# Performance work log

Hardware: AMD Instinct MI355X
Metric: run time of the kernel (lower is better)

The kernel has to match this reference:

```python
import jax, jax.numpy as jnp
import numpy as np

B, N, D, H = 2, 2048, 1024, 16
DH = D // H  # 64


def setup_inputs() -> dict:
    key = jax.random.key(0)
    k1, k2, k3, k4, k5 = jax.random.split(key, 5)
    x = jax.random.normal(k1, (B, N, D), dtype=jnp.float32)
    # per-head kqv Linear weights, stacked: [H, D, 3*DH] (acts as x @ W)
    W_kqv = jax.random.normal(k2, (H, D, 3 * DH), dtype=jnp.float32) * 0.02
    b_kqv = jax.random.normal(k3, (H, 3 * DH), dtype=jnp.float32) * 0.02
    W_proj = jax.random.normal(k4, (D, D), dtype=jnp.float32) * 0.02
    b_proj = jax.random.normal(k5, (D,), dtype=jnp.float32) * 0.02
    return {"x": x, "W_kqv": W_kqv, "b_kqv": b_kqv, "W_proj": W_proj, "b_proj": b_proj}


def reference(x, W_kqv, b_kqv, W_proj, b_proj):
    # per-head projections, all heads batched: [B, H, N, 3*DH]
    kqv = jnp.einsum('bnd,hde->bhne', x, W_kqv) + b_kqv[None, :, None, :]
    # original chunk order is k, q, v
    k, q, v = jnp.split(kqv, 3, axis=-1)  # each [B, H, N, DH]
    # scores: A = q @ k^T / sqrt(DH)  -> [B, H, N, N]
    A = jnp.einsum('bhnd,bhmd->bhnm', q, k) / jnp.sqrt(jnp.asarray(DH, x.dtype))
    causal = jnp.tril(jnp.ones((N, N), dtype=bool))
    A = jnp.where(causal[None, None, :, :], A, -jnp.inf)
    attn = jax.nn.softmax(A, axis=-1)
    sa = jnp.einsum('bhnm,bhmd->bhnd', attn, v)          # [B, H, N, DH]
    sa = sa.transpose(0, 2, 1, 3).reshape(B, N, D)        # concat heads
    out = sa @ W_proj.T + b_proj                          # output projection
    return out
```

## Files before the change

kernel.cpp:

```cpp
#include <hip/hip_runtime.h>
#include <hip/hip_bf16.h>
#include <cstdint>
#include <cstddef>

#define B_  2
#define N_  2048
#define D_  1024
#define H_  16
#define DH_ 64
#define E3_ 192

typedef __attribute__((ext_vector_type(8))) short short8;
typedef __attribute__((ext_vector_type(8))) unsigned short ushort8v;
typedef __attribute__((ext_vector_type(4))) float floatx4;

static __device__ __forceinline__ unsigned short f2bf(float f) {
  union { float f; unsigned u; } c; c.f = f;
  unsigned r = c.u + 0x7fffu + ((c.u >> 16) & 1u);
  return (unsigned short)(r >> 16);
}

#define MFMA(a,b,c) __builtin_amdgcn_mfma_f32_16x16x32_bf16((a),(b),(c),0,0,0)

#define GL_LDS16(g, l) __builtin_amdgcn_global_load_lds( \
    (const __attribute__((address_space(1))) void*)(g),  \
    (__attribute__((address_space(3))) void*)(l), 16, 0, 0)

__global__ __launch_bounds__(256) void k_f2bf(const float* __restrict__ in,
                                              unsigned short* __restrict__ out, int n8) {
  int i = blockIdx.x * blockDim.x + threadIdx.x;
  if (i >= n8) return;
  const float4* p = (const float4*)in + (size_t)i * 2;
  float4 a = p[0], b = p[1];
  ushort8v o;
  o[0]=f2bf(a.x); o[1]=f2bf(a.y); o[2]=f2bf(a.z); o[3]=f2bf(a.w);
  o[4]=f2bf(b.x); o[5]=f2bf(b.y); o[6]=f2bf(b.z); o[7]=f2bf(b.w);
  *((ushort8v*)out + i) = o;
}

__global__ __launch_bounds__(256) void k_twkqv(const float* __restrict__ W,
                                               unsigned short* __restrict__ Wt) {
  __shared__ float tile[64][65];
  int h = blockIdx.z, cat = blockIdx.y, e0 = cat * 64, d0 = blockIdx.x * 64;
  int t = threadIdx.x;
  const float* Wp = W + (size_t)h * D_ * E3_;
  int dr = t >> 2, ec = (t & 3) * 16;
#pragma unroll
  for (int j = 0; j < 16; j += 4) {
    float4 wv = *(const float4*)&Wp[(size_t)(d0 + dr) * E3_ + e0 + ec + j];
    tile[dr][ec + j + 0] = wv.x; tile[dr][ec + j + 1] = wv.y;
    tile[dr][ec + j + 2] = wv.z; tile[dr][ec + j + 3] = wv.w;
  }
  __syncthreads();
  int er = t >> 2, dc = (t & 3) * 16;
  ushort8v o0, o1;
#pragma unroll
  for (int j = 0; j < 8; j++) o0[j] = f2bf(tile[dc + j][er]);
#pragma unroll
  for (int j = 0; j < 8; j++) o1[j] = f2bf(tile[dc + 8 + j][er]);
  size_t o = ((size_t)(cat * 1024 + h * 64 + er)) * D_ + d0 + dc;
  *(ushort8v*)&Wt[o]     = o0;
  *(ushort8v*)&Wt[o + 8] = o1;
}

__global__ __launch_bounds__(256) void k_qkv(const unsigned short* __restrict__ Xb,
                                             const unsigned short* __restrict__ Wt,
                                             const float* __restrict__ bkqv,
                                             unsigned short* __restrict__ Qb,
                                             unsigned short* __restrict__ Kb,
                                             unsigned short* __restrict__ Vt) {
  __shared__ unsigned short Alds[2][128 * 32];
  __shared__ unsigned short Blds[2][128 * 32];
  int t = threadIdx.x;
  int m0 = blockIdx.x * 128, c0 = blockIdx.y * 128;
  int wave = t >> 6, lane = t & 63, quad = lane >> 4, l16 = lane & 15;
  int wm = (wave >> 1) * 64, wn = (wave & 1) * 64;
  floatx4 acc[4][4];
#pragma unroll
  for (int i = 0; i < 4; i++)
#pragma unroll
    for (int j = 0; j < 4; j++) acc[i][j] = (floatx4){0.f, 0.f, 0.f, 0.f};

  const unsigned short* gA = Xb + (size_t)(m0 + wave * 32 + (lane >> 2)) * D_ + (lane & 3) * 8;
  const unsigned short* gB = Wt + (size_t)(c0 + wave * 32 + (lane >> 2)) * D_ + (lane & 3) * 8;
  unsigned short* lA0 = &Alds[0][(wave * 32) * 32];
  unsigned short* lA1 = &Alds[1][(wave * 32) * 32];
  unsigned short* lB0 = &Blds[0][(wave * 32) * 32];
  unsigned short* lB1 = &Blds[1][(wave * 32) * 32];

  for (int k0 = 0; k0 < D_; k0 += 64) {
    GL_LDS16(gA + k0,                 lA0);
    GL_LDS16(gA + k0 + 16 * D_,       lA0 + 16 * 32);
    GL_LDS16(gA + k0 + 32,            lA1);
    GL_LDS16(gA + k0 + 32 + 16 * D_,  lA1 + 16 * 32);
    GL_LDS16(gB + k0,                 lB0);
    GL_LDS16(gB + k0 + 16 * D_,       lB0 + 16 * 32);
    GL_LDS16(gB + k0 + 32,            lB1);
    GL_LDS16(gB + k0 + 32 + 16 * D_,  lB1 + 16 * 32);
    __syncthreads();
#pragma unroll
    for (int kk = 0; kk < 2; kk++) {
      short8 a[4], b[4];
#pragma unroll
      for (int mi = 0; mi < 4; mi++) a[mi] = *(const short8*)&Alds[kk][(wm + mi * 16 + l16) * 32 + quad * 8];
#pragma unroll
      for (int ni = 0; ni < 4; ni++) b[ni] = *(const short8*)&Blds[kk][(wn + ni * 16 + l16) * 32 + quad * 8];
#pragma unroll
      for (int mi = 0; mi < 4; mi++)
#pragma unroll
        for (int ni = 0; ni < 4; ni++) acc[mi][ni] = MFMA(a[mi], b[ni], acc[mi][ni]);
    }
    __syncthreads();
  }

  int cat = c0 >> 10;
#pragma unroll
  for (int mi = 0; mi < 4; mi++)
#pragma unroll
    for (int ni = 0; ni < 4; ni++) {
      int colp = c0 + wn + ni * 16 + l16;
      int h = (colp >> 6) & 15;
      int e = colp & 63;
      int grow = m0 + wm + mi * 16 + quad * 4;
      int b = grow >> 11, n0 = grow & (N_ - 1);
      int bh = b * H_ + h;
      float bias = bkqv[h * E3_ + cat * 64 + e];
      floatx4 v = acc[mi][ni];
      if (cat == 0) {
        size_t base = ((size_t)bh * N_ + n0) * DH_ + e;
#pragma unroll
        for (int r = 0; r < 4; r++) Kb[base + (size_t)r * DH_] = f2bf(v[r] + bias);
      } else if (cat == 1) {
        size_t base = ((size_t)bh * N_ + n0) * DH_ + e;
#pragma unroll
        for (int r = 0; r < 4; r++) Qb[base + (size_t)r * DH_] = f2bf((v[r] + bias) * 0.125f);
      } else {
        ushort4 pk;
        pk.x = f2bf(v[0] + bias); pk.y = f2bf(v[1] + bias);
        pk.z = f2bf(v[2] + bias); pk.w = f2bf(v[3] + bias);
        *(ushort4*)&Vt[((size_t)bh * DH_ + e) * N_ + n0] = pk;
      }
    }
}

#define PSTR 72
__global__ __launch_bounds__(256) void k_flash(const unsigned short* __restrict__ Qb,
                                               const unsigned short* __restrict__ Kb,
                                               const unsigned short* __restrict__ Vt,
                                               unsigned short* __restrict__ sab) {
  int bh = blockIdx.x;
  int yr = blockIdx.y, g = yr >> 3, o = yr & 7;
  int qb = (g == 0) ? o : (g == 1) ? 31 - o : (g == 2) ? 8 + o : 23 - o;
  int q0b = qb * 64;
  int wave = threadIdx.x >> 6;
  int lane = threadIdx.x & 63, quad = lane >> 4, l16 = lane & 15;
  const unsigned short* Qp = Qb + (size_t)bh * N_ * DH_;
  const unsigned short* Kp = Kb + (size_t)bh * N_ * DH_;
  const unsigned short* Vp = Vt + (size_t)bh * DH_ * N_;
  __shared__ unsigned short Klds[2][2 * 64 * 32];
  __shared__ unsigned short Vlds[2][2 * 64 * 32];
  __shared__ unsigned short Plds[4][16 * PSTR];
  unsigned short* P = Plds[wave];

  int q0w = q0b + wave * 16;
  short8 qf0 = *(const short8*)&Qp[(q0w + l16) * DH_ + quad * 8];
  short8 qf1 = *(const short8*)&Qp[(q0w + l16) * DH_ + 32 + quad * 8];

  const unsigned short* gK = Kp + (size_t)(wave * 16 + (lane >> 2)) * DH_ + (lane & 3) * 8;
  const unsigned short* gV = Vp + (size_t)(wave * 16 + (lane >> 2)) * N_ + (lane & 3) * 8;
  int lofs = (wave * 16) * 32;

  floatx4 O[4];
  float lr[4];
#pragma unroll
  for (int r = 0; r < 4; r++) { O[r] = (floatx4){0.f, 0.f, 0.f, 0.f}; lr[r] = 0.f; }

  int nt = (q0b >> 6) + 1;
  GL_LDS16(gK,      &Klds[0][lofs]);
  GL_LDS16(gK + 32, &Klds[0][lofs + 64 * 32]);
  GL_LDS16(gV,      &Vlds[0][lofs]);
  GL_LDS16(gV + 32, &Vlds[0][lofs + 64 * 32]);

  for (int i = 0; i < nt; i++) {
    int buf = i & 1;
    __syncthreads();
    if (i + 1 < nt) {
      int kvn = (i + 1) << 6;
      GL_LDS16(gK + (size_t)kvn * DH_,      &Klds[buf ^ 1][lofs]);
      GL_LDS16(gK + (size_t)kvn * DH_ + 32, &Klds[buf ^ 1][lofs + 64 * 32]);
      GL_LDS16(gV + kvn,                    &Vlds[buf ^ 1][lofs]);
      GL_LDS16(gV + kvn + 32,               &Vlds[buf ^ 1][lofs + 64 * 32]);
    }
    short8 kf[4][2], vf[4][2];
#pragma unroll
    for (int c = 0; c < 4; c++) {
      kf[c][0] = *(const short8*)&Klds[buf][(c * 16 + l16) * 32 + quad * 8];
      kf[c][1] = *(const short8*)&Klds[buf][(64 + c * 16 + l16) * 32 + quad * 8];
      vf[c][0] = *(const short8*)&Vlds[buf][(c * 16 + l16) * 32 + quad * 8];
      vf[c][1] = *(const short8*)&Vlds[buf][(64 + c * 16 + l16) * 32 + quad * 8];
    }
    floatx4 s[4];
#pragma unroll
    for (int c = 0; c < 4; c++) {
      s[c] = (floatx4){0.f, 0.f, 0.f, 0.f};
      s[c] = MFMA(qf0, kf[c][0], s[c]);
      s[c] = MFMA(qf1, kf[c][1], s[c]);
    }
    if (i == nt - 1) {
#pragma unroll
      for (int c = 0; c < 4; c++)
#pragma unroll
        for (int r = 0; r < 4; r++) {
          int row = wave * 16 + quad * 4 + r;
          if (c * 16 + l16 > row) s[c][r] = -1e30f;
        }
    }
#pragma unroll
    for (int c = 0; c < 4; c++)
#pragma unroll
      for (int r = 0; r < 4; r++)
        s[c][r] = __builtin_amdgcn_exp2f(s[c][r] * 1.44269504f);
#pragma unroll
    for (int r = 0; r < 4; r++)
      lr[r] += (s[0][r] + s[1][r]) + (s[2][r] + s[3][r]);
#pragma unroll
    for (int c = 0; c < 4; c++)
#pragma unroll
      for (int r = 0; r < 4; r++)
        P[(quad * 4 + r) * PSTR + c * 16 + l16] = f2bf(s[c][r]);
    __asm__ volatile("s_waitcnt lgkmcnt(0)" ::: "memory");
    short8 pa0 = *(const short8*)&P[l16 * PSTR + quad * 8];
    short8 pa1 = *(const short8*)&P[l16 * PSTR + 32 + quad * 8];
    __asm__ volatile("" ::: "memory");
#pragma unroll
    for (int dt = 0; dt < 4; dt++) {
      O[dt] = MFMA(pa0, vf[dt][0], O[dt]);
      O[dt] = MFMA(pa1, vf[dt][1], O[dt]);
    }
  }
#pragma unroll
  for (int m = 1; m < 16; m <<= 1)
#pragma unroll
    for (int r = 0; r < 4; r++) lr[r] += __shfl_xor(lr[r], m);

  int b = bh >> 4, h = bh & 15;
#pragma unroll
  for (int r = 0; r < 4; r++) {
    float inv = 1.0f / lr[r];
    size_t base = ((size_t)b * N_ + q0w + quad * 4 + r) * D_ + h * DH_;
#pragma unroll
    for (int dt = 0; dt < 4; dt++) sab[base + dt * 16 + l16] = f2bf(O[dt][r] * inv);
  }
}

__global__ __launch_bounds__(256) void k_proj(const unsigned short* __restrict__ sab,
                                              const unsigned short* __restrict__ Wpb,
                                              const float* __restrict__ bproj,
                                              float* __restrict__ out) {
  __shared__ unsigned short Alds[2][128 * 32];
  __shared__ unsigned short Blds[2][64 * 32];
  int t = threadIdx.x;
  int m0 = blockIdx.x * 128, c0 = blockIdx.y * 64;
  int wave = t >> 6, lane = t & 63, quad = lane >> 4, l16 = lane & 15;
  int wm = (wave >> 1) * 64, wn = (wave & 1) * 32;
  floatx4 acc[4][2];
#pragma unroll
  for (int i = 0; i < 4; i++) { acc[i][0] = (floatx4){0,0,0,0}; acc[i][1] = (floatx4){0,0,0,0}; }

  const unsigned short* gA = sab + (size_t)(m0 + wave * 32 + (lane >> 2)) * D_ + (lane & 3) * 8;
  const unsigned short* gB = Wpb + (size_t)(c0 + wave * 16 + (lane >> 2)) * D_ + (lane & 3) * 8;
  unsigned short* lA0 = &Alds[0][(wave * 32) * 32];
  unsigned short* lA1 = &Alds[1][(wave * 32) * 32];
  unsigned short* lB0 = &Blds[0][(wave * 16) * 32];
  unsigned short* lB1 = &Blds[1][(wave * 16) * 32];

  for (int k0 = 0; k0 < D_; k0 += 64) {
    GL_LDS16(gA + k0,                lA0);
    GL_LDS16(gA + k0 + 16 * D_,      lA0 + 16 * 32);
    GL_LDS16(gA + k0 + 32,           lA1);
    GL_LDS16(gA + k0 + 32 + 16 * D_, lA1 + 16 * 32);
    GL_LDS16(gB + k0,                lB0);
    GL_LDS16(gB + k0 + 32,           lB1);
    __syncthreads();
#pragma unroll
    for (int kk = 0; kk < 2; kk++) {
      short8 a[4], b[2];
#pragma unroll
      for (int mi = 0; mi < 4; mi++) a[mi] = *(const short8*)&Alds[kk][(wm + mi * 16 + l16) * 32 + quad * 8];
#pragma unroll
      for (int ni = 0; ni < 2; ni++) b[ni] = *(const short8*)&Blds[kk][(wn + ni * 16 + l16) * 32 + quad * 8];
#pragma unroll
      for (int mi = 0; mi < 4; mi++)
#pragma unroll
        for (int ni = 0; ni < 2; ni++) acc[mi][ni] = MFMA(a[mi], b[ni], acc[mi][ni]);
    }
    __syncthreads();
  }
#pragma unroll
  for (int mi = 0; mi < 4; mi++)
#pragma unroll
    for (int ni = 0; ni < 2; ni++) {
      int col = c0 + wn + ni * 16 + l16;
      int grow = m0 + wm + mi * 16 + quad * 4;
      float bias = bproj[col];
#pragma unroll
      for (int r = 0; r < 4; r++)
        out[(size_t)(grow + r) * D_ + col] = acc[mi][ni][r] + bias;
    }
}

extern "C" void kernel_launch(void* const* d_in, const int* in_sizes, int n_in,
                              void* d_out, int out_size, void* d_ws, size_t ws_size,
                              hipStream_t stream) {
  const float* x     = (const float*)d_in[0];
  const float* Wkqv  = (const float*)d_in[1];
  const float* bkqv  = (const float*)d_in[2];
  const float* Wproj = (const float*)d_in[3];
  const float* bproj = (const float*)d_in[4];
  float* out = (float*)d_out;

  char* w = (char*)d_ws;
  unsigned short* Xb  = (unsigned short*)(w);
  unsigned short* Wt  = (unsigned short*)(w + (8u  << 20));
  unsigned short* Wpb = (unsigned short*)(w + (14u << 20));
  unsigned short* Qb  = (unsigned short*)(w + (16u << 20));
  unsigned short* Kb  = (unsigned short*)(w + (24u << 20));
  unsigned short* Vt  = (unsigned short*)(w + (32u << 20));
  unsigned short* sa  = (unsigned short*)(w + (40u << 20));

  k_f2bf<<<(B_ * N_ * D_ / 8 + 255) / 256, 256, 0, stream>>>(x, Xb, B_ * N_ * D_ / 8);
  k_twkqv<<<dim3(D_ / 64, 3, H_), 256, 0, stream>>>(Wkqv, Wt);
  k_f2bf<<<(D_ * D_ / 8 + 255) / 256, 256, 0, stream>>>(Wproj, Wpb, D_ * D_ / 8);
  k_qkv<<<dim3(B_ * N_ / 128, 3072 / 128), 256, 0, stream>>>(Xb, Wt, bkqv, Qb, Kb, Vt);
  k_flash<<<dim3(B_ * H_, N_ / 64), 256, 0, stream>>>(Qb, Kb, Vt, sa);
  k_proj<<<dim3(B_ * N_ / 128, D_ / 64), 256, 0, stream>>>(sa, Wpb, bproj, out);
}
```

Baseline: 188.6 us.

## Merge prep kernels, double-buffer QKV and proj GEMM loads, shrink proj tiles

```diff
diff --git a/kernel.cpp b/kernel.cpp
--- a/kernel.cpp
+++ b/kernel.cpp
@@ -26,24 +26,30 @@
     (const __attribute__((address_space(1))) void*)(g),  \
     (__attribute__((address_space(3))) void*)(l), 16, 0, 0)
 
-__global__ __launch_bounds__(256) void k_f2bf(const float* __restrict__ in,
-                                              unsigned short* __restrict__ out, int n8) {
-  int i = blockIdx.x * blockDim.x + threadIdx.x;
-  if (i >= n8) return;
-  const float4* p = (const float4*)in + (size_t)i * 2;
-  float4 a = p[0], b = p[1];
-  ushort8v o;
-  o[0]=f2bf(a.x); o[1]=f2bf(a.y); o[2]=f2bf(a.z); o[3]=f2bf(a.w);
-  o[4]=f2bf(b.x); o[5]=f2bf(b.y); o[6]=f2bf(b.z); o[7]=f2bf(b.w);
-  *((ushort8v*)out + i) = o;
-}
-
-__global__ __launch_bounds__(256) void k_twkqv(const float* __restrict__ W,
-                                               unsigned short* __restrict__ Wt) {
+__global__ __launch_bounds__(256) void k_prep(const float* __restrict__ x,
+                                              const float* __restrict__ Wkqv,
+                                              const float* __restrict__ Wproj,
+                                              unsigned short* __restrict__ Xb,
+                                              unsigned short* __restrict__ Wt,
+                                              unsigned short* __restrict__ Wpb) {
   __shared__ float tile[64][65];
-  int h = blockIdx.z, cat = blockIdx.y, e0 = cat * 64, d0 = blockIdx.x * 64;
-  int t = threadIdx.x;
-  const float* Wp = W + (size_t)h * D_ * E3_;
+  int bx = blockIdx.x, t = threadIdx.x;
+  if (bx < 2048 || bx >= 2816) {
+    const float* in = (bx < 2048) ? x : Wproj;
+    unsigned short* out = (bx < 2048) ? Xb : Wpb;
+    int i = ((bx < 2048) ? bx : bx - 2816) * 256 + t;
+    const float4* p = (const float4*)in + (size_t)i * 2;
+    float4 a = p[0], b = p[1];
+    ushort8v o;
+    o[0]=f2bf(a.x); o[1]=f2bf(a.y); o[2]=f2bf(a.z); o[3]=f2bf(a.w);
+    o[4]=f2bf(b.x); o[5]=f2bf(b.y); o[6]=f2bf(b.z); o[7]=f2bf(b.w);
+    *((ushort8v*)out + i) = o;
+    return;
+  }
+  int idx = bx - 2048;
+  int d0 = (idx & 15) * 64, rem = idx >> 4;
+  int cat = rem % 3, h = rem / 3, e0 = cat * 64;
+  const float* Wp = Wkqv + (size_t)h * D_ * E3_;
   int dr = t >> 2, ec = (t & 3) * 16;
 #pragma unroll
   for (int j = 0; j < 16; j += 4) {
@@ -83,34 +89,32 @@
 
   const unsigned short* gA = Xb + (size_t)(m0 + wave * 32 + (lane >> 2)) * D_ + (lane & 3) * 8;
   const unsigned short* gB = Wt + (size_t)(c0 + wave * 32 + (lane >> 2)) * D_ + (lane & 3) * 8;
-  unsigned short* lA0 = &Alds[0][(wave * 32) * 32];
-  unsigned short* lA1 = &Alds[1][(wave * 32) * 32];
-  unsigned short* lB0 = &Blds[0][(wave * 32) * 32];
-  unsigned short* lB1 = &Blds[1][(wave * 32) * 32];
-
-  for (int k0 = 0; k0 < D_; k0 += 64) {
-    GL_LDS16(gA + k0,                 lA0);
-    GL_LDS16(gA + k0 + 16 * D_,       lA0 + 16 * 32);
-    GL_LDS16(gA + k0 + 32,            lA1);
-    GL_LDS16(gA + k0 + 32 + 16 * D_,  lA1 + 16 * 32);
-    GL_LDS16(gB + k0,                 lB0);
-    GL_LDS16(gB + k0 + 16 * D_,       lB0 + 16 * 32);
-    GL_LDS16(gB + k0 + 32,            lB1);
-    GL_LDS16(gB + k0 + 32 + 16 * D_,  lB1 + 16 * 32);
+  int lofs = (wave * 32) * 32;
+
+  GL_LDS16(gA,            &Alds[0][lofs]);
+  GL_LDS16(gA + 16 * D_,  &Alds[0][lofs + 16 * 32]);
+  GL_LDS16(gB,            &Blds[0][lofs]);
+  GL_LDS16(gB + 16 * D_,  &Blds[0][lofs + 16 * 32]);
+
+  for (int i = 0; i < 32; i++) {
+    int buf = i & 1;
     __syncthreads();
-#pragma unroll
-    for (int kk = 0; kk < 2; kk++) {
-      short8 a[4], b[4];
-#pragma unroll
-      for (int mi = 0; mi < 4; mi++) a[mi] = *(const short8*)&Alds[kk][(wm + mi * 16 + l16) * 32 + quad * 8];
-#pragma unroll
-      for (int ni = 0; ni < 4; ni++) b[ni] = *(const short8*)&Blds[kk][(wn + ni * 16 + l16) * 32 + quad * 8];
-#pragma unroll
-      for (int mi = 0; mi < 4; mi++)
-#pragma unroll
-        for (int ni = 0; ni < 4; ni++) acc[mi][ni] = MFMA(a[mi], b[ni], acc[mi][ni]);
-    }
-    __syncthreads();
+    if (i + 1 < 32) {
+      int k0 = (i + 1) * 32;
+      GL_LDS16(gA + k0,            &Alds[buf ^ 1][lofs]);
+      GL_LDS16(gA + k0 + 16 * D_,  &Alds[buf ^ 1][lofs + 16 * 32]);
+      GL_LDS16(gB + k0,            &Blds[buf ^ 1][lofs]);
+      GL_LDS16(gB + k0 + 16 * D_,  &Blds[buf ^ 1][lofs + 16 * 32]);
+    }
+    short8 a[4], b[4];
+#pragma unroll
+    for (int mi = 0; mi < 4; mi++) a[mi] = *(const short8*)&Alds[buf][(wm + mi * 16 + l16) * 32 + quad * 8];
+#pragma unroll
+    for (int ni = 0; ni < 4; ni++) b[ni] = *(const short8*)&Blds[buf][(wn + ni * 16 + l16) * 32 + quad * 8];
+#pragma unroll
+    for (int mi = 0; mi < 4; mi++)
+#pragma unroll
+      for (int ni = 0; ni < 4; ni++) acc[mi][ni] = MFMA(a[mi], b[ni], acc[mi][ni]);
   }
 
   int cat = c0 >> 10;
@@ -257,47 +261,50 @@
                                               const unsigned short* __restrict__ Wpb,
                                               const float* __restrict__ bproj,
                                               float* __restrict__ out) {
-  __shared__ unsigned short Alds[2][128 * 32];
-  __shared__ unsigned short Blds[2][64 * 32];
+  __shared__ unsigned short Alds[2][2][64 * 32];
+  __shared__ unsigned short Blds[2][2][64 * 32];
   int t = threadIdx.x;
-  int m0 = blockIdx.x * 128, c0 = blockIdx.y * 64;
+  int m0 = blockIdx.x * 64, c0 = blockIdx.y * 64;
   int wave = t >> 6, lane = t & 63, quad = lane >> 4, l16 = lane & 15;
-  int wm = (wave >> 1) * 64, wn = (wave & 1) * 32;
-  floatx4 acc[4][2];
-#pragma unroll
-  for (int i = 0; i < 4; i++) { acc[i][0] = (floatx4){0,0,0,0}; acc[i][1] = (floatx4){0,0,0,0}; }
-
-  const unsigned short* gA = sab + (size_t)(m0 + wave * 32 + (lane >> 2)) * D_ + (lane & 3) * 8;
+  int wm = (wave >> 1) * 32, wn = (wave & 1) * 32;
+  floatx4 acc[2][2];
+#pragma unroll
+  for (int i = 0; i < 2; i++) { acc[i][0] = (floatx4){0,0,0,0}; acc[i][1] = (floatx4){0,0,0,0}; }
+
+  const unsigned short* gA = sab + (size_t)(m0 + wave * 16 + (lane >> 2)) * D_ + (lane & 3) * 8;
   const unsigned short* gB = Wpb + (size_t)(c0 + wave * 16 + (lane >> 2)) * D_ + (lane & 3) * 8;
-  unsigned short* lA0 = &Alds[0][(wave * 32) * 32];
-  unsigned short* lA1 = &Alds[1][(wave * 32) * 32];
-  unsigned short* lB0 = &Blds[0][(wave * 16) * 32];
-  unsigned short* lB1 = &Blds[1][(wave * 16) * 32];
-
-  for (int k0 = 0; k0 < D_; k0 += 64) {
-    GL_LDS16(gA + k0,                lA0);
-    GL_LDS16(gA + k0 + 16 * D_,      lA0 + 16 * 32);
-    GL_LDS16(gA + k0 + 32,           lA1);
-    GL_LDS16(gA + k0 + 32 + 16 * D_, lA1 + 16 * 32);
-    GL_LDS16(gB + k0,                lB0);
-    GL_LDS16(gB + k0 + 32,           lB1);
+  int lofs = (wave * 16) * 32;
+
+  GL_LDS16(gA,      &Alds[0][0][lofs]);
+  GL_LDS16(gA + 32, &Alds[0][1][lofs]);
+  GL_LDS16(gB,      &Blds[0][0][lofs]);
+  GL_LDS16(gB + 32, &Blds[0][1][lofs]);
+
+  for (int i = 0; i < 16; i++) {
+    int buf = i & 1;
     __syncthreads();
+    if (i + 1 < 16) {
+      int k0 = (i + 1) * 64;
+      GL_LDS16(gA + k0,      &Alds[buf ^ 1][0][lofs]);
+      GL_LDS16(gA + k0 + 32, &Alds[buf ^ 1][1][lofs]);
+      GL_LDS16(gB + k0,      &Blds[buf ^ 1][0][lofs]);
+      GL_LDS16(gB + k0 + 32, &Blds[buf ^ 1][1][lofs]);
+    }
 #pragma unroll
     for (int kk = 0; kk < 2; kk++) {
-      short8 a[4], b[2];
-#pragma unroll
-      for (int mi = 0; mi < 4; mi++) a[mi] = *(const short8*)&Alds[kk][(wm + mi * 16 + l16) * 32 + quad * 8];
-#pragma unroll
-      for (int ni = 0; ni < 2; ni++) b[ni] = *(const short8*)&Blds[kk][(wn + ni * 16 + l16) * 32 + quad * 8];
-#pragma unroll
-      for (int mi = 0; mi < 4; mi++)
+      short8 a[2], b[2];
+#pragma unroll
+      for (int mi = 0; mi < 2; mi++) a[mi] = *(const short8*)&Alds[buf][kk][(wm + mi * 16 + l16) * 32 + quad * 8];
+#pragma unroll
+      for (int ni = 0; ni < 2; ni++) b[ni] = *(const short8*)&Blds[buf][kk][(wn + ni * 16 + l16) * 32 + quad * 8];
+#pragma unroll
+      for (int mi = 0; mi < 2; mi++)
 #pragma unroll
         for (int ni = 0; ni < 2; ni++) acc[mi][ni] = MFMA(a[mi], b[ni], acc[mi][ni]);
     }
-    __syncthreads();
-  }
-#pragma unroll
-  for (int mi = 0; mi < 4; mi++)
+  }
+#pragma unroll
+  for (int mi = 0; mi < 2; mi++)
 #pragma unroll
     for (int ni = 0; ni < 2; ni++) {
       int col = c0 + wn + ni * 16 + l16;
@@ -328,10 +335,8 @@
   unsigned short* Vt  = (unsigned short*)(w + (32u << 20));
   unsigned short* sa  = (unsigned short*)(w + (40u << 20));
 
-  k_f2bf<<<(B_ * N_ * D_ / 8 + 255) / 256, 256, 0, stream>>>(x, Xb, B_ * N_ * D_ / 8);
-  k_twkqv<<<dim3(D_ / 64, 3, H_), 256, 0, stream>>>(Wkqv, Wt);
-  k_f2bf<<<(D_ * D_ / 8 + 255) / 256, 256, 0, stream>>>(Wproj, Wpb, D_ * D_ / 8);
+  k_prep<<<2048 + 768 + 512, 256, 0, stream>>>(x, Wkqv, Wproj, Xb, Wt, Wpb);
   k_qkv<<<dim3(B_ * N_ / 128, 3072 / 128), 256, 0, stream>>>(Xb, Wt, bkqv, Qb, Kb, Vt);
   k_flash<<<dim3(B_ * H_, N_ / 64), 256, 0, stream>>>(Qb, Kb, Vt, sa);
-  k_proj<<<dim3(B_ * N_ / 128, D_ / 64), 256, 0, stream>>>(sa, Wpb, bproj, out);
-}
+  k_proj<<<dim3(B_ * N_ / 64, D_ / 64), 256, 0, stream>>>(sa, Wpb, bproj, out);
+}
```

Measured after the change: 185.7 us. No clear change (-1.5%).
